# Kernel tuning notes

Hardware: AMD Instinct MI355X
Metric: run time of the kernel (lower is better)

The kernel has to match this reference:

```python
import jax, jax.numpy as jnp
import numpy as np

K = 3   # up_kernel
S = 2   # scale_factor per stage
COMP = 64  # compressed channels (mmcv CARAFEPack default)


def _conv2d(x, w, b, pad):
    y = jax.lax.conv_general_dilated(
        x, w, window_strides=(1, 1), padding=[(pad, pad), (pad, pad)],
        dimension_numbers=('NCHW', 'OIHW', 'NCHW'))
    return y + b[None, :, None, None]


def _carafe_stage(x, wc, bc, we, be):
    B, C, H, W = x.shape
    # kernel prediction branch
    comp = _conv2d(x, wc, bc, 0)                 # [B, 64, H, W]
    m = _conv2d(comp, we, be, 1)                 # [B, K*K*S*S, H, W]
    # pixel shuffle: [B, K*K, S, S, H, W] -> [B, K*K, H, S, W, S]
    m = m.reshape(B, K * K, S, S, H, W).transpose(0, 1, 4, 2, 5, 3)
    # softmax over the K*K kernel weights per output pixel
    m = jax.nn.softmax(m, axis=1)                # [B, 9, H, S, W, S]
    # 3x3 neighborhoods of source (row-major kernel order, matching mmcv)
    xp = jnp.pad(x, ((0, 0), (0, 0), (1, 1), (1, 1)))
    patches = jnp.stack(
        [xp[:, :, dy:dy + H, dx:dx + W] for dy in range(K) for dx in range(K)],
        axis=2)                                   # [B, C, 9, H, W]
    # content-aware reassembly: weights shared across channels (up_group=1)
    out = jnp.einsum('bckhw,bkhpwq->bchpwq', patches, m)
    return out.reshape(B, C, S * H, S * W)


def setup_inputs() -> dict:
    key = jax.random.key(0)
    ks = jax.random.split(key, 12)
    B, C, H, W = 2, 256, 16, 16
    inp = {
        'source': jax.random.normal(ks[0], (B, C, H, W), jnp.float32),
        'guidance': jax.random.normal(ks[1], (B, 3, 256, 256), jnp.float32),
    }
    sc = 1.0 / np.sqrt(C)        # fan-in of 1x1 compressor
    se = 1.0 / np.sqrt(COMP * K * K)  # fan-in of 3x3 encoder
    for i in range(4):
        inp[f'wc{i+1}'] = jax.random.normal(ks[2 + 2 * i], (COMP, C, 1, 1), jnp.float32) * sc
        inp[f'bc{i+1}'] = jnp.zeros((COMP,), jnp.float32)
        inp[f'we{i+1}'] = jax.random.normal(ks[3 + 2 * i], (K * K * S * S, COMP, K, K), jnp.float32) * se
        inp[f'be{i+1}'] = jnp.zeros((K * K * S * S,), jnp.float32)
    return inp


def reference(source, guidance,
              wc1, bc1, we1, be1,
              wc2, bc2, we2, be2,
              wc3, bc3, we3, be3,
              wc4, bc4, we4, be4):
    x = _carafe_stage(source, wc1, bc1, we1, be1)
    x = _carafe_stage(x, wc2, bc2, we2, be2)
    x = _carafe_stage(x, wc3, bc3, we3, be3)
    x = _carafe_stage(x, wc4, bc4, we4, be4)
    return x
```

## Files before the change

### kernel.cpp

```cpp
#include <hip/hip_runtime.h>

#define LB __launch_bounds__(256)

__global__ LB void prep_weights(
    const float* __restrict__ wcA, const float* __restrict__ wcB,
    const float* __restrict__ wcC, const float* __restrict__ wcD,
    const float* __restrict__ weA, const float* __restrict__ weB,
    const float* __restrict__ weC, const float* __restrict__ weD,
    float* __restrict__ wcT, float* __restrict__ weT)
{
    int seg = blockIdx.y;
    int t = blockIdx.x * 256 + threadIdx.x;
    if (seg < 4) {
        if (t >= 64 * 256) return;
        const float* w = (seg == 0) ? wcA : (seg == 1) ? wcB : (seg == 2) ? wcC : wcD;
        int c = t & 255, o = t >> 8;
        wcT[seg * 16384 + ((o >> 3) * 256 + c) * 8 + (o & 7)] = w[t];
    } else {
        if (t >= 36 * 64 * 9) return;
        const float* w = (seg == 4) ? weA : (seg == 5) ? weB : (seg == 6) ? weC : weD;
        int kt = t % 9;
        int r = t / 9;
        int i = r & 63;
        int o = r >> 6;
        int kk = o >> 2, pq = o & 3;
        weT[(seg - 4) * 36864 + ((pq * 64 + i) * 9 + kt) * 16 + kk] = w[t];
    }
}

template<int PPT>
__global__ LB void compress_k(const float* __restrict__ x, const float* __restrict__ wcT,
                              const float* __restrict__ bc, float* __restrict__ comp, int lgW)
{
    const int lgHW = 2 * lgW;
    const int HW = 1 << lgHW;
    const int og = blockIdx.y;
    int tid = blockIdx.x * 256 + threadIdx.x;
    int pix = tid * PPT;
    int b = pix >> lgHW;
    int hw = pix & (HW - 1);
    const float* xp = x + (((size_t)b * 256) << lgHW) + hw;
    const float* wr = wcT + og * 2048;

    float acc[8][PPT];
    #pragma unroll
    for (int j = 0; j < 8; j++) {
        float bv = bc[og * 8 + j];
        #pragma unroll
        for (int p = 0; p < PPT; p++) acc[j][p] = bv;
    }

    #pragma unroll 4
    for (int c = 0; c < 256; c++) {
        float xv[PPT];
        if (PPT == 1) {
            xv[0] = xp[(size_t)c << lgHW];
        } else {
            float2 t2 = *(const float2*)(xp + ((size_t)c << lgHW));
            xv[0] = t2.x; xv[1] = t2.y;
        }
        const float* w8 = wr + c * 8;
        #pragma unroll
        for (int j = 0; j < 8; j++) {
            float wv = w8[j];
            #pragma unroll
            for (int p = 0; p < PPT; p++) acc[j][p] += wv * xv[p];
        }
    }

    float* op = comp + (((size_t)b * 64 + og * 8) << lgHW) + hw;
    #pragma unroll
    for (int j = 0; j < 8; j++) {
        if (PPT == 1) {
            op[(size_t)j << lgHW] = acc[j][0];
        } else {
            *(float2*)(op + ((size_t)j << lgHW)) = make_float2(acc[j][0], acc[j][1]);
        }
    }
}

__global__ LB void encoder_k(const float* __restrict__ comp, const float* __restrict__ weT,
                             const float* __restrict__ be, float* __restrict__ mnorm, int lgW)
{
    const int lgHW = 2 * lgW;
    const int HW = 1 << lgHW, W = 1 << lgW, H = W;
    int idx = blockIdx.x * 256 + threadIdx.x;
    int pq = __builtin_amdgcn_readfirstlane(idx >> (lgHW + 1));
    int pix = idx & (2 * HW - 1);
    int b = pix >> lgHW;
    int hw = pix & (HW - 1);
    int h = hw >> lgW, w = hw & (W - 1);

    int off[9];
    float msk[9];
    #pragma unroll
    for (int ky = 0; ky < 3; ky++) {
        int ys = h + ky - 1;
        bool yok = (unsigned)ys < (unsigned)H;
        #pragma unroll
        for (int kx = 0; kx < 3; kx++) {
            int xs = w + kx - 1;
            bool ok = yok && ((unsigned)xs < (unsigned)W);
            int kt = ky * 3 + kx;
            off[kt] = ok ? ((ys << lgW) + xs) : 0;
            msk[kt] = ok ? 1.f : 0.f;
        }
    }

    float acc[9];
    #pragma unroll
    for (int kk = 0; kk < 9; kk++) acc[kk] = be[kk * 4 + pq];

    const float* wp = weT + pq * 9216;
    const float* cb = comp + (((size_t)b) << lgHW) * 64;
    #pragma unroll 2
    for (int i = 0; i < 64; i++) {
        const float* ci = cb + ((size_t)i << lgHW);
        float tap[9];
        #pragma unroll
        for (int kt = 0; kt < 9; kt++) tap[kt] = ci[off[kt]] * msk[kt];
        const float* wi = wp + i * 144;
        #pragma unroll
        for (int kt = 0; kt < 9; kt++) {
            const float* wt = wi + kt * 16;
            float4 w0 = *(const float4*)(wt);
            float4 w1 = *(const float4*)(wt + 4);
            float  w8 = wt[8];
            float tv = tap[kt];
            acc[0] += w0.x * tv; acc[1] += w0.y * tv; acc[2] += w0.z * tv;
            acc[3] += w0.w * tv; acc[4] += w1.x * tv; acc[5] += w1.y * tv;
            acc[6] += w1.z * tv; acc[7] += w1.w * tv; acc[8] += w8 * tv;
        }
    }

    float m = acc[0];
    #pragma unroll
    for (int kk = 1; kk < 9; kk++) m = fmaxf(m, acc[kk]);
    float s = 0.f;
    #pragma unroll
    for (int kk = 0; kk < 9; kk++) { acc[kk] = __expf(acc[kk] - m); s += acc[kk]; }
    float r = 1.f / s;
    float* mp = mnorm + (((size_t)b * 36) << lgHW) + hw;
    #pragma unroll
    for (int kk = 0; kk < 9; kk++) mp[(size_t)(kk * 4 + pq) << lgHW] = acc[kk] * r;
}

template<int CPT>
__global__ LB void reassembly_k(const float* __restrict__ x, const float* __restrict__ mnorm,
                                float* __restrict__ out, int lgW)
{
    const int lgHW = 2 * lgW;
    const int HW = 1 << lgHW, W = 1 << lgW, H = W;
    int lane = threadIdx.x & 63;
    int cg = threadIdx.x >> 6;
    int nbsh = lgHW - 5;
    int pb = blockIdx.x & ((1 << nbsh) - 1);
    int cs = blockIdx.x >> nbsh;
    int pix = pb * 64 + lane;
    int b = pix >> lgHW;
    int hw = pix & (HW - 1);
    int h = hw >> lgW, w = hw & (W - 1);

    int off[9];
    float msk[9];
    #pragma unroll
    for (int ky = 0; ky < 3; ky++) {
        int ys = h + ky - 1;
        bool yok = (unsigned)ys < (unsigned)H;
        #pragma unroll
        for (int kx = 0; kx < 3; kx++) {
            int xs = w + kx - 1;
            bool ok = yok && ((unsigned)xs < (unsigned)W);
            int kt = ky * 3 + kx;
            off[kt] = ok ? ((ys << lgW) + xs) : 0;
            msk[kt] = ok ? 1.f : 0.f;
        }
    }
    const float* mp = mnorm + (((size_t)b * 36) << lgHW) + hw;
    float wreg[36];
    #pragma unroll
    for (int ch = 0; ch < 36; ch++) wreg[ch] = mp[(size_t)ch << lgHW];

    int c0 = (cs * 4 + cg) * CPT;
    const float* xb = x + ((size_t)b * 256 + c0) * HW;
    size_t OW = (size_t)W * 2;
    float* ob = out + (((size_t)b * 256 + c0) * 2 * H + 2 * h) * OW + 2 * w;
    #pragma unroll 2
    for (int it = 0; it < CPT; it++) {
        const float* xc = xb + ((size_t)it << lgHW);
        float a00 = 0.f, a01 = 0.f, a10 = 0.f, a11 = 0.f;
        #pragma unroll
        for (int kt = 0; kt < 9; kt++) {
            float tap = xc[off[kt]] * msk[kt];
            a00 += tap * wreg[kt * 4 + 0];
            a01 += tap * wreg[kt * 4 + 1];
            a10 += tap * wreg[kt * 4 + 2];
            a11 += tap * wreg[kt * 4 + 3];
        }
        float* oc = ob + (size_t)it * 2 * H * OW;
        *(float2*)oc = make_float2(a00, a01);
        *(float2*)(oc + OW) = make_float2(a10, a11);
    }
}

extern "C" void kernel_launch(void* const* d_in, const int* in_sizes, int n_in,
                              void* d_out, int out_size, void* d_ws, size_t ws_size,
                              hipStream_t stream)
{
    const float* src = (const float*)d_in[0];
    const float* wc[4]; const float* bc[4]; const float* we[4]; const float* be[4];
    for (int s = 0; s < 4; s++) {
        wc[s] = (const float*)d_in[2 + 4 * s];
        bc[s] = (const float*)d_in[3 + 4 * s];
        we[s] = (const float*)d_in[4 + 4 * s];
        be[s] = (const float*)d_in[5 + 4 * s];
    }
    float* ws   = (float*)d_ws;
    float* x1   = ws;
    float* x2   = x1 + 524288;
    float* x3   = x2 + 2097152;
    float* comp = x3 + 8388608;
    float* mn   = comp + 2097152;
    float* wcT  = mn + 1179648;
    float* weT  = wcT + 65536;

    prep_weights<<<dim3(81, 8), 256, 0, stream>>>(
        wc[0], wc[1], wc[2], wc[3], we[0], we[1], we[2], we[3], wcT, weT);

    const float* xin = src;
    float* stage_out[4] = {x1, x2, x3, (float*)d_out};
    int lgW = 4;
    for (int s = 0; s < 4; s++) {
        int HW = 1 << (2 * lgW);
        int npix = 2 * HW;
        if (s < 2)
            compress_k<1><<<dim3(npix / 256, 8), 256, 0, stream>>>(
                xin, wcT + s * 16384, bc[s], comp, lgW);
        else
            compress_k<2><<<dim3(npix / 512, 8), 256, 0, stream>>>(
                xin, wcT + s * 16384, bc[s], comp, lgW);
        encoder_k<<<npix >> 6, 256, 0, stream>>>(comp, weT + s * 36864, be[s], mn, lgW);
        int nb = npix >> 6;
        if (s < 2)
            reassembly_k<4><<<nb * 16, 256, 0, stream>>>(xin, mn, stage_out[s], lgW);
        else
            reassembly_k<16><<<nb * 4, 256, 0, stream>>>(xin, mn, stage_out[s], lgW);
        xin = stage_out[s];
        lgW++;
    }
}
```

Baseline: 534.1 us.

## Remap compressor and encoder threads for reuse, enlarge reassembly channel batches

The 1x1 compressor now runs one wavefront per 16-channel output group, with 64 pixels per block. Each thread accumulates 16 outputs from float4 weight loads, using a new channel-major weight layout. The encoder gives each of a block's four wavefronts one sub-pixel position for the same 64 pixels, so they share reads of the compressed features. Reassembly processes more channels per thread (16 for the early stages, 64 for the later ones), which cuts the number of blocks and the repeated loading of mask weights, at the cost of less grid parallelism.

```diff
diff --git a/kernel.cpp b/kernel.cpp
--- a/kernel.cpp
+++ b/kernel.cpp
@@ -15,7 +15,7 @@
         if (t >= 64 * 256) return;
         const float* w = (seg == 0) ? wcA : (seg == 1) ? wcB : (seg == 2) ? wcC : wcD;
         int c = t & 255, o = t >> 8;
-        wcT[seg * 16384 + ((o >> 3) * 256 + c) * 8 + (o & 7)] = w[t];
+        wcT[seg * 16384 + c * 64 + o] = w[t];
     } else {
         if (t >= 36 * 64 * 9) return;
         const float* w = (seg == 4) ? weA : (seg == 5) ? weB : (seg == 6) ? weC : weD;
@@ -28,55 +28,39 @@
     }
 }
 
-template<int PPT>
 __global__ LB void compress_k(const float* __restrict__ x, const float* __restrict__ wcT,
                               const float* __restrict__ bc, float* __restrict__ comp, int lgW)
 {
     const int lgHW = 2 * lgW;
     const int HW = 1 << lgHW;
-    const int og = blockIdx.y;
-    int tid = blockIdx.x * 256 + threadIdx.x;
-    int pix = tid * PPT;
+    int lane = threadIdx.x & 63;
+    int og = __builtin_amdgcn_readfirstlane(threadIdx.x >> 6);
+    int pix = blockIdx.x * 64 + lane;
     int b = pix >> lgHW;
     int hw = pix & (HW - 1);
     const float* xp = x + (((size_t)b * 256) << lgHW) + hw;
-    const float* wr = wcT + og * 2048;
-
-    float acc[8][PPT];
-    #pragma unroll
-    for (int j = 0; j < 8; j++) {
-        float bv = bc[og * 8 + j];
-        #pragma unroll
-        for (int p = 0; p < PPT; p++) acc[j][p] = bv;
-    }
-
-    #pragma unroll 4
+    const float* wr = wcT + og * 16;
+
+    float acc[16];
+    #pragma unroll
+    for (int j = 0; j < 16; j++) acc[j] = bc[og * 16 + j];
+
+    #pragma unroll 2
     for (int c = 0; c < 256; c++) {
-        float xv[PPT];
-        if (PPT == 1) {
-            xv[0] = xp[(size_t)c << lgHW];
-        } else {
-            float2 t2 = *(const float2*)(xp + ((size_t)c << lgHW));
-            xv[0] = t2.x; xv[1] = t2.y;
-        }
-        const float* w8 = wr + c * 8;
-        #pragma unroll
-        for (int j = 0; j < 8; j++) {
-            float wv = w8[j];
-            #pragma unroll
-            for (int p = 0; p < PPT; p++) acc[j][p] += wv * xv[p];
-        }
-    }
-
-    float* op = comp + (((size_t)b * 64 + og * 8) << lgHW) + hw;
-    #pragma unroll
-    for (int j = 0; j < 8; j++) {
-        if (PPT == 1) {
-            op[(size_t)j << lgHW] = acc[j][0];
-        } else {
-            *(float2*)(op + ((size_t)j << lgHW)) = make_float2(acc[j][0], acc[j][1]);
-        }
-    }
+        float xv = xp[(size_t)c << lgHW];
+        const float* w = wr + c * 64;
+        float wv[16];
+        *(float4*)&wv[0]  = *(const float4*)(w);
+        *(float4*)&wv[4]  = *(const float4*)(w + 4);
+        *(float4*)&wv[8]  = *(const float4*)(w + 8);
+        *(float4*)&wv[12] = *(const float4*)(w + 12);
+        #pragma unroll
+        for (int j = 0; j < 16; j++) acc[j] += wv[j] * xv;
+    }
+
+    float* op = comp + (((size_t)b * 64 + og * 16) << lgHW) + hw;
+    #pragma unroll
+    for (int j = 0; j < 16; j++) op[(size_t)j << lgHW] = acc[j];
 }
 
 __global__ LB void encoder_k(const float* __restrict__ comp, const float* __restrict__ weT,
@@ -84,9 +68,9 @@
 {
     const int lgHW = 2 * lgW;
     const int HW = 1 << lgHW, W = 1 << lgW, H = W;
-    int idx = blockIdx.x * 256 + threadIdx.x;
-    int pq = __builtin_amdgcn_readfirstlane(idx >> (lgHW + 1));
-    int pix = idx & (2 * HW - 1);
+    int lane = threadIdx.x & 63;
+    int pq = __builtin_amdgcn_readfirstlane(threadIdx.x >> 6);
+    int pix = blockIdx.x * 64 + lane;
     int b = pix >> lgHW;
     int hw = pix & (HW - 1);
     int h = hw >> lgW, w = hw & (W - 1);
@@ -233,18 +217,13 @@
     for (int s = 0; s < 4; s++) {
         int HW = 1 << (2 * lgW);
         int npix = 2 * HW;
+        int nb = npix >> 6;
+        compress_k<<<nb, 256, 0, stream>>>(xin, wcT + s * 16384, bc[s], comp, lgW);
+        encoder_k<<<nb, 256, 0, stream>>>(comp, weT + s * 36864, be[s], mn, lgW);
         if (s < 2)
-            compress_k<1><<<dim3(npix / 256, 8), 256, 0, stream>>>(
-                xin, wcT + s * 16384, bc[s], comp, lgW);
+            reassembly_k<16><<<nb * 4, 256, 0, stream>>>(xin, mn, stage_out[s], lgW);
         else
-            compress_k<2><<<dim3(npix / 512, 8), 256, 0, stream>>>(
-                xin, wcT + s * 16384, bc[s], comp, lgW);
-        encoder_k<<<npix >> 6, 256, 0, stream>>>(comp, weT + s * 36864, be[s], mn, lgW);
-        int nb = npix >> 6;
-        if (s < 2)
-            reassembly_k<4><<<nb * 16, 256, 0, stream>>>(xin, mn, stage_out[s], lgW);
-        else
-            reassembly_k<16><<<nb * 4, 256, 0, stream>>>(xin, mn, stage_out[s], lgW);
+            reassembly_k<64><<<nb, 256, 0, stream>>>(xin, mn, stage_out[s], lgW);
         xin = stage_out[s];
         lgW++;
     }
```

After: 639.4 us. 1.2x slower.
